# Optimization experiments

Hardware: AMD Instinct MI355X
Metric: run time of the kernel (lower is better)

The kernel has to match this reference:

```python
import jax, jax.numpy as jnp
import numpy as np
import math

N_NODES = 100_000
N_EDGES = 800_000
NODE_DIM = 128
EDGE_DIM = 64
HIDDEN = 128
HEADS = 8
HEAD_DIM = HIDDEN // HEADS


def _segment_softmax(scores, seg, n):
    # scores: [E, H], grouped by destination node `seg`
    m = jax.ops.segment_max(scores, seg, num_segments=n)
    e = jnp.exp(scores - m[seg])
    d = jax.ops.segment_sum(e, seg, num_segments=n)
    return e / d[seg]


def _layer_norm(x, g, b, eps=1e-5):
    mu = jnp.mean(x, axis=-1, keepdims=True)
    var = jnp.mean((x - mu) ** 2, axis=-1, keepdims=True)
    return (x - mu) * jax.lax.rsqrt(var + eps) * g + b


def _graph_conv(x, row, col, edge_proj, Wn, b, n):
    # PyG GraphConvolution: add self-loops, symmetric deg normalization,
    # msg = (Wn x)[row] + edge_lin(edge_attr); aggregate (add) at col.
    # Self-loop edges carry zero edge features (edge_lin has no bias -> contributes 0).
    loop = jnp.arange(n)
    row2 = jnp.concatenate([row, loop])
    col2 = jnp.concatenate([col, loop])
    ep2 = jnp.concatenate([edge_proj, jnp.zeros((n, edge_proj.shape[1]), edge_proj.dtype)])
    deg = jax.ops.segment_sum(jnp.ones_like(col2, x.dtype), col2, num_segments=n)
    dinv = jnp.where(deg > 0, jax.lax.rsqrt(jnp.maximum(deg, 1e-12)), 0.0)
    norm = dinv[row2] * dinv[col2]
    h = x @ Wn                                   # [n, hidden]
    msg = (h[row2] + ep2) * norm[:, None]        # [E+n, hidden]
    return jax.ops.segment_sum(msg, col2, num_segments=n) + b


def setup_inputs() -> dict:
    key = jax.random.key(0)
    ks = jax.random.split(key, 20)

    def xav(k, shape):
        fan_in, fan_out = shape[0], shape[-1]
        s = math.sqrt(2.0 / (fan_in + fan_out))
        return jax.random.normal(k, shape, jnp.float32) * s

    return {
        "x": jax.random.normal(ks[0], (N_NODES, NODE_DIM), jnp.float32),
        "edge_index": jax.random.randint(ks[1], (2, N_EDGES), 0, N_NODES, jnp.int64),
        "edge_attr": jax.random.normal(ks[2], (N_EDGES, EDGE_DIM), jnp.float32),
        "W_qkv": xav(ks[3], (NODE_DIM, 3 * HIDDEN)),
        "b_qkv": jnp.zeros((3 * HIDDEN,), jnp.float32),
        "W_ek": xav(ks[4], (EDGE_DIM, HIDDEN)),
        "b_ek": jnp.zeros((HIDDEN,), jnp.float32),
        "W_n1": xav(ks[5], (NODE_DIM, HIDDEN)),
        "W_e1": xav(ks[6], (EDGE_DIM, HIDDEN)),
        "b1": jnp.zeros((HIDDEN,), jnp.float32),
        "W_n2": xav(ks[7], (HIDDEN, HIDDEN)),
        "W_e2": xav(ks[8], (EDGE_DIM, HIDDEN)),
        "b2": jnp.zeros((HIDDEN,), jnp.float32),
        "W_out": xav(ks[9], (HIDDEN, NODE_DIM)),
        "b_out": jnp.zeros((NODE_DIM,), jnp.float32),
        "ln_g": jnp.ones((NODE_DIM,), jnp.float32),
        "ln_b": jnp.zeros((NODE_DIM,), jnp.float32),
    }


def reference(x, edge_index, edge_attr, W_qkv, b_qkv, W_ek, b_ek,
              W_n1, W_e1, b1, W_n2, W_e2, b2, W_out, b_out, ln_g, ln_b):
    n = x.shape[0]
    row, col = edge_index[0], edge_index[1]

    # --- compute_dynamic_edges (computed in the original forward but its
    # result is discarded; kept here for fidelity to the source math) ---
    qkv = x @ W_qkv + b_qkv
    q, k, _v = jnp.split(qkv, 3, axis=-1)
    q = q.reshape(n, HEADS, HEAD_DIM)
    k = k.reshape(n, HEADS, HEAD_DIM)
    ek = (edge_attr @ W_ek + b_ek).reshape(-1, HEADS, HEAD_DIM)
    scores = jnp.sum(q[row] * (k[col] + ek), axis=-1) / math.sqrt(HEAD_DIM)  # [E, H]
    _edge_weights = _segment_softmax(scores, col, n)  # unused downstream (as in source)

    # --- two GraphConvolution layers (dropout is identity in eval mode) ---
    h1 = jax.nn.gelu(_graph_conv(x, row, col, edge_attr @ W_e1, W_n1, b1, n), approximate=False)
    h2 = jax.nn.gelu(_graph_conv(h1, row, col, edge_attr @ W_e2, W_n2, b2, n), approximate=False)

    out = h2 @ W_out + b_out
    return _layer_norm(out + x, ln_g, ln_b)
```

## Files before the change

### kernel.cpp

```cpp
#include <hip/hip_runtime.h>
#include <math.h>

#define N_NODES 100000
#define N_EDGES 800000
#define NBLK 391

__global__ void k_count(const int* __restrict__ col, int* __restrict__ cnt) {
    int e = blockIdx.x * 256 + threadIdx.x;
    if (e < N_EDGES) {
        unsigned c = (unsigned)col[e];
        if (c < N_NODES) atomicAdd(&cnt[c], 1);
    }
}

__global__ void k_blocksum(const int* __restrict__ cnt, int* __restrict__ bsum) {
    __shared__ int sc[256];
    int t = threadIdx.x, i = blockIdx.x * 256 + t;
    sc[t] = (i < N_NODES) ? cnt[i] : 0;
    __syncthreads();
    for (int o = 128; o; o >>= 1) {
        if (t < o) sc[t] += sc[t + o];
        __syncthreads();
    }
    if (t == 0) bsum[blockIdx.x] = sc[0];
}

__global__ void k_scanblocks(const int* __restrict__ bsum, int* __restrict__ bexcl) {
    if (threadIdx.x == 0) {
        int run = 0;
        for (int b = 0; b < NBLK; b++) { bexcl[b] = run; run += bsum[b]; }
    }
}

__global__ void k_offsets(const int* __restrict__ cnt, const int* __restrict__ bexcl,
                          int* __restrict__ off, int* __restrict__ pos) {
    __shared__ int sc[256];
    int t = threadIdx.x, i = blockIdx.x * 256 + t;
    int v = (i < N_NODES) ? cnt[i] : 0;
    sc[t] = v;
    __syncthreads();
    for (int o = 1; o < 256; o <<= 1) {
        int tv = (t >= o) ? sc[t - o] : 0;
        __syncthreads();
        sc[t] += tv;
        __syncthreads();
    }
    if (i < N_NODES) {
        int s = bexcl[blockIdx.x] + (sc[t] - v);
        off[i] = s;
        pos[i] = s;
    }
}

__global__ void k_dinv(const int* __restrict__ cnt, float* __restrict__ dinv) {
    int i = blockIdx.x * 256 + threadIdx.x;
    if (i < N_NODES) dinv[i] = rsqrtf((float)(cnt[i] + 1));
}

__global__ void k_build(const int* __restrict__ row, const int* __restrict__ col,
                        int* __restrict__ pos, const float* __restrict__ dinv,
                        int* __restrict__ srcE, int* __restrict__ eidE,
                        float* __restrict__ dinvE) {
    int e = blockIdx.x * 256 + threadIdx.x;
    if (e < N_EDGES) {
        unsigned r = (unsigned)row[e], c = (unsigned)col[e];
        if (r < N_NODES && c < N_NODES) {
            int slot = atomicAdd(&pos[c], 1);
            srcE[slot] = (int)r;
            eidE[slot] = e;
            if (dinvE) dinvE[slot] = dinv[r];
        }
    }
}

__global__ __launch_bounds__(256) void k_gather(
    const float* __restrict__ X, const float* __restrict__ EAraw,
    const int* __restrict__ off, const int* __restrict__ cnt,
    const int* __restrict__ srcE, const int* __restrict__ eidE,
    const float* __restrict__ dinvE, const float* __restrict__ dinv,
    float* __restrict__ act, int mode)
{
    int w = threadIdx.x >> 6, l = threadIdx.x & 63;
    int c = blockIdx.x * 4 + w;
    if (c >= N_NODES) return;
    int beg = off[c], d = cnt[c];
    const float2* X2 = (const float2*)X;
    float a0 = 0.f, a1 = 0.f, ae = 0.f;

    int j = 0;
    for (; j + 4 <= d; j += 4) {
        int s0 = srcE[beg + j],     s1 = srcE[beg + j + 1];
        int s2 = srcE[beg + j + 2], s3 = srcE[beg + j + 3];
        float v0 = dinvE[beg + j],     v1 = dinvE[beg + j + 1];
        float v2 = dinvE[beg + j + 2], v3 = dinvE[beg + j + 3];
        float2 x0 = X2[(size_t)s0 * 64 + l];
        float2 x1 = X2[(size_t)s1 * 64 + l];
        float2 x2 = X2[(size_t)s2 * 64 + l];
        float2 x3 = X2[(size_t)s3 * 64 + l];
        a0 += v0 * x0.x + v1 * x1.x + v2 * x2.x + v3 * x3.x;
        a1 += v0 * x0.y + v1 * x1.y + v2 * x2.y + v3 * x3.y;
        if (mode == 0) {
            int e0 = eidE[beg + j],     e1 = eidE[beg + j + 1];
            int e2 = eidE[beg + j + 2], e3 = eidE[beg + j + 3];
            float q0 = EAraw[(size_t)e0 * 64 + l];
            float q1 = EAraw[(size_t)e1 * 64 + l];
            float q2 = EAraw[(size_t)e2 * 64 + l];
            float q3 = EAraw[(size_t)e3 * 64 + l];
            ae += v0 * q0 + v1 * q1 + v2 * q2 + v3 * q3;
        }
    }
    for (; j < d; j++) {
        int s = srcE[beg + j];
        float v = dinvE[beg + j];
        float2 xv = X2[(size_t)s * 64 + l];
        a0 += v * xv.x;
        a1 += v * xv.y;
        if (mode == 0) ae += v * EAraw[(size_t)eidE[beg + j] * 64 + l];
    }

    float dv = dinv[c], dv2 = dv * dv;
    float2 xc = X2[(size_t)c * 64 + l];
    float* arow = act + (size_t)c * 192;
    ((float2*)arow)[l] = make_float2(dv * a0 + dv2 * xc.x, dv * a1 + dv2 * xc.y);
    if (mode == 0) arow[128 + l] = dv * ae;
}

__global__ __launch_bounds__(256, 3) void k_gemm(
    const float* __restrict__ act,
    const float* __restrict__ Wn, const float* __restrict__ We,
    const float* __restrict__ bias, float* __restrict__ out)
{
    __shared__ float sact[64][192];
    int t = threadIdx.x;
    int w = t >> 6, l = t & 63;

    const size_t CAP = (size_t)N_NODES * 192;
    size_t base = (size_t)blockIdx.x * (64 * 192);
    #pragma unroll
    for (int i = 0; i < 12; i++) {
        size_t fi = base + (size_t)(i * 256 + t) * 4;
        float4 v = make_float4(0.f, 0.f, 0.f, 0.f);
        if (fi + 4 <= CAP) v = *(const float4*)(act + fi);
        *(float4*)&sact[0][(i * 256 + t) * 4] = v;
    }
    __syncthreads();

    int row0 = blockIdx.x * 64 + w * 16;
    float acc[16][2] = {};

    const float2* Wn2 = (const float2*)Wn;
    for (int k = 0; k < 128; k += 4) {
        float2 w0 = Wn2[(k + 0) * 64 + l];
        float2 w1 = Wn2[(k + 1) * 64 + l];
        float2 w2 = Wn2[(k + 2) * 64 + l];
        float2 w3 = Wn2[(k + 3) * 64 + l];
        #pragma unroll
        for (int r = 0; r < 16; r++) {
            float4 a = *(const float4*)&sact[w * 16 + r][k];
            acc[r][0] += a.x * w0.x + a.y * w1.x + a.z * w2.x + a.w * w3.x;
            acc[r][1] += a.x * w0.y + a.y * w1.y + a.z * w2.y + a.w * w3.y;
        }
    }

    const float2* We2 = (const float2*)We;
    for (int k = 0; k < 64; k += 4) {
        float2 w0 = We2[(k + 0) * 64 + l];
        float2 w1 = We2[(k + 1) * 64 + l];
        float2 w2 = We2[(k + 2) * 64 + l];
        float2 w3 = We2[(k + 3) * 64 + l];
        #pragma unroll
        for (int r = 0; r < 16; r++) {
            float4 a = *(const float4*)&sact[w * 16 + r][128 + k];
            acc[r][0] += a.x * w0.x + a.y * w1.x + a.z * w2.x + a.w * w3.x;
            acc[r][1] += a.x * w0.y + a.y * w1.y + a.z * w2.y + a.w * w3.y;
        }
    }

    float2 bb = ((const float2*)bias)[l];
    #pragma unroll
    for (int r = 0; r < 16; r++) {
        int c = row0 + r;
        if (c >= N_NODES) break;
        float v0 = acc[r][0] + bb.x;
        float v1 = acc[r][1] + bb.y;
        v0 = 0.5f * v0 * (1.0f + erff(v0 * 0.70710678f));
        v1 = 0.5f * v1 * (1.0f + erff(v1 * 0.70710678f));
        ((float2*)out)[(size_t)c * 64 + l] = make_float2(v0, v1);
    }
}

__global__ __launch_bounds__(256) void k_layer(
    const float* __restrict__ X, const float* __restrict__ EAraw,
    const float* __restrict__ EaIn, float* __restrict__ EaOut,
    const int* __restrict__ off, const int* __restrict__ cnt,
    const int* __restrict__ srcE, const int* __restrict__ eidE,
    const float* __restrict__ dinv,
    const float* __restrict__ Wn, const float* __restrict__ We,
    const float* __restrict__ bias, float* __restrict__ out, int mode)
{
    __shared__ float act[4][4][192];
    int w = threadIdx.x >> 6, l = threadIdx.x & 63;
    int row0 = blockIdx.x * 16 + w * 4;

    for (int r = 0; r < 4; r++) {
        int c = row0 + r;
        int beg = off[c];
        int d = cnt[c];
        float a0 = 0.f, a1 = 0.f, ae = 0.f;
        for (int j = 0; j < d; j++) {
            unsigned s = (unsigned)srcE[beg + j];
            if (s >= N_NODES) continue;
            float sv = dinv[s];
            float2 xv = ((const float2*)X)[s * 64 + l];
            a0 += sv * xv.x;
            a1 += sv * xv.y;
            if (mode == 0) {
                unsigned e = (unsigned)eidE[beg + j];
                if (e < N_EDGES) ae += sv * EAraw[e * 64 + l];
            }
        }
        float dv = dinv[c], dv2 = dv * dv;
        float2 xc = ((const float2*)X)[c * 64 + l];
        act[w][r][2 * l]     = dv * a0 + dv2 * xc.x;
        act[w][r][2 * l + 1] = dv * a1 + dv2 * xc.y;
        if (mode == 0) {
            act[w][r][128 + l] = dv * ae;
            EaOut[c * 64 + l] = ae;
        } else {
            act[w][r][128 + l] = dv * EaIn[c * 64 + l];
        }
    }
    __syncthreads();

    float acc[4][2] = {};
    for (int k = 0; k < 128; k++) {
        float2 wv = ((const float2*)Wn)[k * 64 + l];
        #pragma unroll
        for (int r = 0; r < 4; r++) {
            float a = act[w][r][k];
            acc[r][0] += a * wv.x;
            acc[r][1] += a * wv.y;
        }
    }
    for (int k = 0; k < 64; k++) {
        float2 wv = ((const float2*)We)[k * 64 + l];
        #pragma unroll
        for (int r = 0; r < 4; r++) {
            float a = act[w][r][128 + k];
            acc[r][0] += a * wv.x;
            acc[r][1] += a * wv.y;
        }
    }

    float2 bb = ((const float2*)bias)[l];
    for (int r = 0; r < 4; r++) {
        float v0 = acc[r][0] + bb.x;
        float v1 = acc[r][1] + bb.y;
        v0 = 0.5f * v0 * (1.0f + erff(v0 * 0.70710678f));
        v1 = 0.5f * v1 * (1.0f + erff(v1 * 0.70710678f));
        ((float2*)out)[(row0 + r) * 64 + l] = make_float2(v0, v1);
    }
}

__global__ __launch_bounds__(256) void k_final(
    const float* __restrict__ h2, const float* __restrict__ x,
    const float* __restrict__ Wo, const float* __restrict__ bo,
    const float* __restrict__ g, const float* __restrict__ lb,
    float* __restrict__ out)
{
    __shared__ float lds[4][4][128];
    int w = threadIdx.x >> 6, l = threadIdx.x & 63;
    int row0 = blockIdx.x * 16 + w * 4;

    for (int r = 0; r < 4; r++) {
        int c = row0 + r;
        float2 hv = ((const float2*)h2)[(size_t)c * 64 + l];
        lds[w][r][2 * l]     = hv.x;
        lds[w][r][2 * l + 1] = hv.y;
    }
    __syncthreads();

    float acc[4][2] = {};
    const float2* Wo2 = (const float2*)Wo;
    for (int k = 0; k < 128; k += 4) {
        float2 w0 = Wo2[(k + 0) * 64 + l];
        float2 w1 = Wo2[(k + 1) * 64 + l];
        float2 w2 = Wo2[(k + 2) * 64 + l];
        float2 w3 = Wo2[(k + 3) * 64 + l];
        #pragma unroll
        for (int r = 0; r < 4; r++) {
            float4 a = *(const float4*)&lds[w][r][k];
            acc[r][0] += a.x * w0.x + a.y * w1.x + a.z * w2.x + a.w * w3.x;
            acc[r][1] += a.x * w0.y + a.y * w1.y + a.z * w2.y + a.w * w3.y;
        }
    }

    float2 bov = ((const float2*)bo)[l];
    float2 gv  = ((const float2*)g)[l];
    float2 lbv = ((const float2*)lb)[l];

    for (int r = 0; r < 4; r++) {
        int c = row0 + r;
        float2 xv = ((const float2*)x)[(size_t)c * 64 + l];
        float v0 = acc[r][0] + bov.x + xv.x;
        float v1 = acc[r][1] + bov.y + xv.y;
        float s = v0 + v1;
        #pragma unroll
        for (int o = 32; o; o >>= 1) s += __shfl_xor(s, o, 64);
        float mu = s * (1.0f / 128.0f);
        float d0 = v0 - mu, d1 = v1 - mu;
        float sq = d0 * d0 + d1 * d1;
        #pragma unroll
        for (int o = 32; o; o >>= 1) sq += __shfl_xor(sq, o, 64);
        float rs = rsqrtf(sq * (1.0f / 128.0f) + 1e-5f);
        float2 ov;
        ov.x = d0 * rs * gv.x + lbv.x;
        ov.y = d1 * rs * gv.y + lbv.y;
        ((float2*)out)[(size_t)c * 64 + l] = ov;
    }
}

extern "C" void kernel_launch(void* const* d_in, const int* in_sizes, int n_in,
                              void* d_out, int out_size, void* d_ws, size_t ws_size,
                              hipStream_t stream)
{
    const float* x   = (const float*)d_in[0];
    const int*   ei  = (const int*)d_in[1];
    const float* ea  = (const float*)d_in[2];
    const float* Wn1 = (const float*)d_in[7];
    const float* We1 = (const float*)d_in[8];
    const float* b1  = (const float*)d_in[9];
    const float* Wn2 = (const float*)d_in[10];
    const float* We2 = (const float*)d_in[11];
    const float* b2  = (const float*)d_in[12];
    const float* Wo  = (const float*)d_in[13];
    const float* bo  = (const float*)d_in[14];
    const float* lng = (const float*)d_in[15];
    const float* lnb = (const float*)d_in[16];
    const int* row = ei;
    const int* col = ei + N_EDGES;

    char* ws = (char*)d_ws;
    size_t off_b = 0;
    auto alloc = [&](size_t bytes) {
        void* p = ws + off_b;
        off_b += (bytes + 255) & ~(size_t)255;
        return p;
    };
    int*   cnt   = (int*)  alloc((size_t)N_NODES * 4);
    int*   off   = (int*)  alloc((size_t)N_NODES * 4);
    int*   pos   = (int*)  alloc((size_t)N_NODES * 4);
    int*   bsum  = (int*)  alloc((size_t)NBLK * 4);
    int*   bexcl = (int*)  alloc((size_t)NBLK * 4);
    float* dinv  = (float*)alloc((size_t)N_NODES * 4);
    int*   srcE  = (int*)  alloc((size_t)N_EDGES * 4);
    int*   eidE  = (int*)  alloc((size_t)N_EDGES * 4);
    float* h1    = (float*)alloc((size_t)N_NODES * 128 * 4);
    size_t common_end = off_b;

    float* dinvE = (float*)alloc((size_t)N_EDGES * 4);
    float* act   = (float*)alloc((size_t)N_NODES * 192 * 4);
    size_t split_end = off_b;

    float* Ea = (float*)(ws + common_end);
    size_t fused_end = common_end + (((size_t)N_NODES * 64 * 4 + 255) & ~(size_t)255);

    bool use_split = (split_end <= ws_size);
    if (!use_split && fused_end > ws_size) return;

    float* h2 = (float*)d_out;

    hipMemsetAsync(cnt, 0, (size_t)N_NODES * 4, stream);

    k_count     <<<(N_EDGES + 255) / 256, 256, 0, stream>>>(col, cnt);
    k_blocksum  <<<NBLK, 256, 0, stream>>>(cnt, bsum);
    k_scanblocks<<<1, 64, 0, stream>>>(bsum, bexcl);
    k_offsets   <<<NBLK, 256, 0, stream>>>(cnt, bexcl, off, pos);
    k_dinv      <<<NBLK, 256, 0, stream>>>(cnt, dinv);
    k_build     <<<(N_EDGES + 255) / 256, 256, 0, stream>>>(
        row, col, pos, dinv, srcE, eidE, use_split ? dinvE : nullptr);

    if (use_split) {
        k_gather<<<N_NODES / 4, 256, 0, stream>>>(x, ea, off, cnt, srcE, eidE,
                                                  dinvE, dinv, act, 0);
        k_gemm  <<<(N_NODES + 63) / 64, 256, 0, stream>>>(act, Wn1, We1, b1, h1);
        k_gather<<<N_NODES / 4, 256, 0, stream>>>(h1, nullptr, off, cnt, srcE, eidE,
                                                  dinvE, dinv, act, 1);
        k_gemm  <<<(N_NODES + 63) / 64, 256, 0, stream>>>(act, Wn2, We2, b2, h2);
    } else {
        k_layer<<<N_NODES / 16, 256, 0, stream>>>(x, ea, nullptr, Ea,
                                                  off, cnt, srcE, eidE, dinv,
                                                  Wn1, We1, b1, h1, 0);
        k_layer<<<N_NODES / 16, 256, 0, stream>>>(h1, nullptr, Ea, nullptr,
                                                  off, cnt, srcE, eidE, dinv,
                                                  Wn2, We2, b2, h2, 1);
    }
    k_final<<<N_NODES / 16, 256, 0, stream>>>(h2, x, Wo, bo, lng, lnb, (float*)d_out);
}
```

Baseline: 896.6 us.

## Prefetch first 16 neighbors in gather, template mode, parallelize block scan

The gather kernel now issues loads for the first 16 neighbor indices, weights, feature rows and edge rows up front, with zero weights past the degree and clamped indices, so many independent memory requests are in flight at once. Mode becomes a template parameter and offset/count are packed into one int2 load. The serial single-thread block-offset scan is replaced with a parallel shared-memory scan. The cost is wasted loads for low-degree nodes, which reads past each node's edges (hence padding the edge arrays), plus higher register pressure.

```diff
diff --git a/kernel.cpp b/kernel.cpp
--- a/kernel.cpp
+++ b/kernel.cpp
@@ -26,14 +26,22 @@
 }
 
 __global__ void k_scanblocks(const int* __restrict__ bsum, int* __restrict__ bexcl) {
-    if (threadIdx.x == 0) {
-        int run = 0;
-        for (int b = 0; b < NBLK; b++) { bexcl[b] = run; run += bsum[b]; }
-    }
+    __shared__ int s[512];
+    int t = threadIdx.x;
+    s[t] = (t < NBLK) ? bsum[t] : 0;
+    __syncthreads();
+    for (int o = 1; o < 512; o <<= 1) {
+        int v = (t >= o) ? s[t - o] : 0;
+        __syncthreads();
+        s[t] += v;
+        __syncthreads();
+    }
+    if (t < NBLK) bexcl[t] = t ? s[t - 1] : 0;
 }
 
 __global__ void k_offsets(const int* __restrict__ cnt, const int* __restrict__ bexcl,
-                          int* __restrict__ off, int* __restrict__ pos) {
+                          int* __restrict__ off, int* __restrict__ pos,
+                          int2* __restrict__ offcnt) {
     __shared__ int sc[256];
     int t = threadIdx.x, i = blockIdx.x * 256 + t;
     int v = (i < N_NODES) ? cnt[i] : 0;
@@ -49,6 +57,7 @@
         int s = bexcl[blockIdx.x] + (sc[t] - v);
         off[i] = s;
         pos[i] = s;
+        if (offcnt) offcnt[i] = make_int2(s, v);
     }
 }
 
@@ -73,56 +82,75 @@
     }
 }
 
+template<int MODE>
 __global__ __launch_bounds__(256) void k_gather(
     const float* __restrict__ X, const float* __restrict__ EAraw,
-    const int* __restrict__ off, const int* __restrict__ cnt,
+    const int2* __restrict__ offcnt,
     const int* __restrict__ srcE, const int* __restrict__ eidE,
     const float* __restrict__ dinvE, const float* __restrict__ dinv,
-    float* __restrict__ act, int mode)
+    float* __restrict__ act)
 {
     int w = threadIdx.x >> 6, l = threadIdx.x & 63;
     int c = blockIdx.x * 4 + w;
     if (c >= N_NODES) return;
-    int beg = off[c], d = cnt[c];
+    int2 oc = offcnt[c];
+    int beg = oc.x, d = oc.y;
     const float2* X2 = (const float2*)X;
+
+    int sU[16]; float vU[16]; int eU[16];
+    #pragma unroll
+    for (int i = 0; i < 16; i++) sU[i] = srcE[beg + i];
+    #pragma unroll
+    for (int i = 0; i < 16; i++) vU[i] = dinvE[beg + i];
+    if (MODE == 0) {
+        #pragma unroll
+        for (int i = 0; i < 16; i++) eU[i] = eidE[beg + i];
+    }
+    #pragma unroll
+    for (int i = 0; i < 16; i++) {
+        if (i >= d) vU[i] = 0.f;
+        sU[i] = ((unsigned)sU[i] < N_NODES) ? sU[i] : 0;
+        if (MODE == 0) eU[i] = ((unsigned)eU[i] < N_EDGES) ? eU[i] : 0;
+    }
+
+    float2 xv[16];
+    #pragma unroll
+    for (int i = 0; i < 16; i++) xv[i] = X2[(size_t)sU[i] * 64 + l];
+    float ev[16];
+    if (MODE == 0) {
+        #pragma unroll
+        for (int i = 0; i < 16; i++) ev[i] = EAraw[(size_t)eU[i] * 64 + l];
+    }
+
     float a0 = 0.f, a1 = 0.f, ae = 0.f;
-
-    int j = 0;
-    for (; j + 4 <= d; j += 4) {
-        int s0 = srcE[beg + j],     s1 = srcE[beg + j + 1];
-        int s2 = srcE[beg + j + 2], s3 = srcE[beg + j + 3];
-        float v0 = dinvE[beg + j],     v1 = dinvE[beg + j + 1];
-        float v2 = dinvE[beg + j + 2], v3 = dinvE[beg + j + 3];
-        float2 x0 = X2[(size_t)s0 * 64 + l];
-        float2 x1 = X2[(size_t)s1 * 64 + l];
-        float2 x2 = X2[(size_t)s2 * 64 + l];
-        float2 x3 = X2[(size_t)s3 * 64 + l];
-        a0 += v0 * x0.x + v1 * x1.x + v2 * x2.x + v3 * x3.x;
-        a1 += v0 * x0.y + v1 * x1.y + v2 * x2.y + v3 * x3.y;
-        if (mode == 0) {
-            int e0 = eidE[beg + j],     e1 = eidE[beg + j + 1];
-            int e2 = eidE[beg + j + 2], e3 = eidE[beg + j + 3];
-            float q0 = EAraw[(size_t)e0 * 64 + l];
-            float q1 = EAraw[(size_t)e1 * 64 + l];
-            float q2 = EAraw[(size_t)e2 * 64 + l];
-            float q3 = EAraw[(size_t)e3 * 64 + l];
-            ae += v0 * q0 + v1 * q1 + v2 * q2 + v3 * q3;
-        }
-    }
-    for (; j < d; j++) {
+    float b0 = 0.f, b1 = 0.f, be = 0.f;
+    #pragma unroll
+    for (int i = 0; i < 16; i += 2) {
+        a0 += vU[i] * xv[i].x;
+        a1 += vU[i] * xv[i].y;
+        b0 += vU[i + 1] * xv[i + 1].x;
+        b1 += vU[i + 1] * xv[i + 1].y;
+        if (MODE == 0) {
+            ae += vU[i] * ev[i];
+            be += vU[i + 1] * ev[i + 1];
+        }
+    }
+    a0 += b0; a1 += b1; ae += be;
+
+    for (int j = 16; j < d; j++) {
         int s = srcE[beg + j];
         float v = dinvE[beg + j];
-        float2 xv = X2[(size_t)s * 64 + l];
-        a0 += v * xv.x;
-        a1 += v * xv.y;
-        if (mode == 0) ae += v * EAraw[(size_t)eidE[beg + j] * 64 + l];
+        float2 x = X2[(size_t)s * 64 + l];
+        a0 += v * x.x;
+        a1 += v * x.y;
+        if (MODE == 0) ae += v * EAraw[(size_t)eidE[beg + j] * 64 + l];
     }
 
     float dv = dinv[c], dv2 = dv * dv;
     float2 xc = X2[(size_t)c * 64 + l];
     float* arow = act + (size_t)c * 192;
     ((float2*)arow)[l] = make_float2(dv * a0 + dv2 * xc.x, dv * a1 + dv2 * xc.y);
-    if (mode == 0) arow[128 + l] = dv * ae;
+    if (MODE == 0) arow[128 + l] = dv * ae;
 }
 
 __global__ __launch_bounds__(256, 3) void k_gemm(
@@ -353,13 +381,14 @@
     int*   bsum  = (int*)  alloc((size_t)NBLK * 4);
     int*   bexcl = (int*)  alloc((size_t)NBLK * 4);
     float* dinv  = (float*)alloc((size_t)N_NODES * 4);
-    int*   srcE  = (int*)  alloc((size_t)N_EDGES * 4);
-    int*   eidE  = (int*)  alloc((size_t)N_EDGES * 4);
+    int*   srcE  = (int*)  alloc((size_t)(N_EDGES + 16) * 4);
+    int*   eidE  = (int*)  alloc((size_t)(N_EDGES + 16) * 4);
     float* h1    = (float*)alloc((size_t)N_NODES * 128 * 4);
     size_t common_end = off_b;
 
-    float* dinvE = (float*)alloc((size_t)N_EDGES * 4);
-    float* act   = (float*)alloc((size_t)N_NODES * 192 * 4);
+    float* dinvE  = (float*)alloc((size_t)(N_EDGES + 16) * 4);
+    int2*  offcnt = (int2*) alloc((size_t)N_NODES * 8);
+    float* act    = (float*)alloc((size_t)N_NODES * 192 * 4);
     size_t split_end = off_b;
 
     float* Ea = (float*)(ws + common_end);
@@ -374,18 +403,19 @@
 
     k_count     <<<(N_EDGES + 255) / 256, 256, 0, stream>>>(col, cnt);
     k_blocksum  <<<NBLK, 256, 0, stream>>>(cnt, bsum);
-    k_scanblocks<<<1, 64, 0, stream>>>(bsum, bexcl);
-    k_offsets   <<<NBLK, 256, 0, stream>>>(cnt, bexcl, off, pos);
+    k_scanblocks<<<1, 512, 0, stream>>>(bsum, bexcl);
+    k_offsets   <<<NBLK, 256, 0, stream>>>(cnt, bexcl, off, pos,
+                                           use_split ? offcnt : nullptr);
     k_dinv      <<<NBLK, 256, 0, stream>>>(cnt, dinv);
     k_build     <<<(N_EDGES + 255) / 256, 256, 0, stream>>>(
         row, col, pos, dinv, srcE, eidE, use_split ? dinvE : nullptr);
 
     if (use_split) {
-        k_gather<<<N_NODES / 4, 256, 0, stream>>>(x, ea, off, cnt, srcE, eidE,
-                                                  dinvE, dinv, act, 0);
+        k_gather<0><<<(N_NODES + 3) / 4, 256, 0, stream>>>(x, ea, offcnt,
+                                                           srcE, eidE, dinvE, dinv, act);
         k_gemm  <<<(N_NODES + 63) / 64, 256, 0, stream>>>(act, Wn1, We1, b1, h1);
-        k_gather<<<N_NODES / 4, 256, 0, stream>>>(h1, nullptr, off, cnt, srcE, eidE,
-                                                  dinvE, dinv, act, 1);
+        k_gather<1><<<(N_NODES + 3) / 4, 256, 0, stream>>>(h1, nullptr, offcnt,
+                                                           srcE, eidE, dinvE, dinv, act);
         k_gemm  <<<(N_NODES + 63) / 64, 256, 0, stream>>>(act, Wn2, We2, b2, h2);
     } else {
         k_layer<<<N_NODES / 16, 256, 0, stream>>>(x, ea, nullptr, Ea,
```

After: 943.7 us. 1.05x slower.
